# Kernel tuning notes

Measured on AMD Instinct MI355X. Metric: run time of the kernel, lower is better.

## Reference

```python
import jax, jax.numpy as jnp
import numpy as np

B, S, DIM, H = 2, 2048, 1024, 16
DK = DIM // H  # 64
NEG = -10000000000.0


def setup_inputs() -> dict:
    key = jax.random.key(0)
    k1, k2, k3, k4, k5, k6 = jax.random.split(key, 6)
    dec_xs = jax.random.normal(k1, (B, S, DIM), dtype=jnp.float32)
    enc_xs = jax.random.normal(k2, (B, S, DIM), dtype=jnp.float32)
    mask = jax.random.randint(k3, (B, S, S), 0, 2, dtype=jnp.int32)
    # torch Linear weights: out = x @ W.T, bias=False
    sc = 1.0 / np.sqrt(DIM)
    Wq = jax.random.normal(k4, (DIM, DIM), dtype=jnp.float32) * sc
    Wkv = jax.random.normal(k5, (2 * DIM, DIM), dtype=jnp.float32) * sc
    Wo = jax.random.normal(k6, (DIM, DIM), dtype=jnp.float32) * sc
    return {"dec_xs": dec_xs, "enc_xs": enc_xs, "Wq": Wq, "Wkv": Wkv, "Wo": Wo, "mask": mask}


def reference(dec_xs, enc_xs, Wq, Wkv, Wo, mask):
    b, s, dim = enc_xs.shape
    qs = dec_xs @ Wq.T                      # [b,s,dim]  (dropout inactive in eval)
    kv = enc_xs @ Wkv.T                     # [b,s,2*dim]
    ks, vs = jnp.split(kv, 2, axis=-1)
    # head layout: view(b, s, dk, h) -- heads LAST, as in the original
    qs = qs.reshape(b, s, DK, H)
    ks = ks.reshape(b, s, DK, H)
    vs = vs.reshape(b, s, DK, H)
    scores = jnp.einsum('bqdh,bkdh->bqkh', qs, ks) / np.sqrt(DK)
    scores = jnp.where(mask[..., None] == 0, NEG, scores)
    weights = jax.nn.softmax(scores, axis=-2)  # softmax over key axis
    out = jnp.einsum('bqkh,bkdh->bqdh', weights, vs).reshape(b, s, dim)
    return out @ Wo.T
```

## Files before the change

kernel.cpp:

```cpp
#include <hip/hip_runtime.h>
#include <hip/hip_bf16.h>

#define BB 2
#define SS 2048
#define DIMM 1024
#define HH 16
#define DKK 64
#define QSCALE 0.18033688011112042592f

using bf16 = __hip_bfloat16;
typedef __attribute__((ext_vector_type(8))) short v8s;
typedef __attribute__((ext_vector_type(4))) short v4s;
typedef __attribute__((ext_vector_type(4))) float f32x4;

__device__ __forceinline__ void cvt4(const float* __restrict__ s,
                                     bf16* __restrict__ d, int idx) {
  const float4 f = ((const float4*)s)[idx];
  bf16 t[4] = {__float2bfloat16(f.x), __float2bfloat16(f.y),
               __float2bfloat16(f.z), __float2bfloat16(f.w)};
  *(v4s*)(d + (size_t)idx * 4) = *(const v4s*)t;
}

__global__ __launch_bounds__(256) void convert_pack_kernel(
    const float* __restrict__ dec, const float* __restrict__ enc,
    const float* __restrict__ Wq, const float* __restrict__ Wkv,
    const float* __restrict__ Wo, const int* __restrict__ mask,
    bf16* __restrict__ decb, bf16* __restrict__ encb, bf16* __restrict__ Wqb,
    bf16* __restrict__ Wkvb, bf16* __restrict__ Wob,
    unsigned long long* __restrict__ mp) {
  const int gid = blockIdx.x * 256 + threadIdx.x;
  const int NT = 256 * 1024;
#pragma unroll
  for (int i = 0; i < 4; ++i) cvt4(dec, decb, gid + i * NT);
#pragma unroll
  for (int i = 0; i < 4; ++i) cvt4(enc, encb, gid + i * NT);
  cvt4(Wq, Wqb, gid);
#pragma unroll
  for (int i = 0; i < 2; ++i) cvt4(Wkv, Wkvb, gid + i * NT);
  cvt4(Wo, Wob, gid);
  const int lane = threadIdx.x & 63;
  const int wave_id = gid >> 6;
  for (int i = 0; i < 32; ++i) {
    const size_t w = (size_t)wave_id * 32 + i;
    const unsigned long long bm = __ballot(mask[w * 64 + lane] != 0);
    if (lane == 0) mp[w] = bm;
  }
}

__global__ __launch_bounds__(256) void proj_gemm_kernel(
    const bf16* __restrict__ decb, const bf16* __restrict__ encb,
    const bf16* __restrict__ Wqb, const bf16* __restrict__ Wkvb,
    bf16* __restrict__ Qr, bf16* __restrict__ Kr, bf16* __restrict__ Vt) {
  __shared__ __align__(16) bf16 As[128][72];
  __shared__ __align__(16) bf16 Bs[128][72];
  const int t = threadIdx.x;
  const int wave = t >> 6, lane = t & 63;
  const int quad = lane >> 4, l15 = lane & 15;
  const int wm = (wave >> 1) * 64, wn = (wave & 1) * 64;
  const int bx = blockIdx.x;
  const int kind = bx >> 3;
  const int g = bx & 7;
  const int m0 = blockIdx.y * 128;

  const bf16* Asrc = (kind == 0) ? decb : encb;
  const bf16* Wsrc = (kind == 0) ? Wqb : Wkvb;

  const int sr = t >> 2;
  const int sc = (t & 3) * 16;
  const int wr0 = sr * 16 + g * 2 + ((kind == 2) ? DIMM : 0);
  const int wr1 = sr * 16 + g * 2 + 1 + ((kind == 2) ? DIMM : 0);

  v8s apf[4], bpf[4];
  auto loadA = [&](int kc) {
    const bf16* p0 = Asrc + (size_t)(m0 + sr) * DIMM + kc + sc;
    apf[0] = ((const v8s*)p0)[0];
    apf[1] = ((const v8s*)p0)[1];
    const bf16* p1 = Asrc + (size_t)(m0 + sr + 64) * DIMM + kc + sc;
    apf[2] = ((const v8s*)p1)[0];
    apf[3] = ((const v8s*)p1)[1];
  };
  auto loadB = [&](int kc) {
    const bf16* q0 = Wsrc + (size_t)wr0 * DIMM + kc + sc;
    bpf[0] = ((const v8s*)q0)[0];
    bpf[1] = ((const v8s*)q0)[1];
    const bf16* q1 = Wsrc + (size_t)wr1 * DIMM + kc + sc;
    bpf[2] = ((const v8s*)q1)[0];
    bpf[3] = ((const v8s*)q1)[1];
  };

  f32x4 acc[4][4] = {};
  loadA(0);
  loadB(0);

  for (int kc = 0; kc < DIMM; kc += 64) {
    __syncthreads();
    *(v8s*)&As[sr][sc] = apf[0];
    *(v8s*)&As[sr][sc + 8] = apf[1];
    *(v8s*)&As[sr + 64][sc] = apf[2];
    *(v8s*)&As[sr + 64][sc + 8] = apf[3];
    *(v8s*)&Bs[sr][sc] = bpf[0];
    *(v8s*)&Bs[sr][sc + 8] = bpf[1];
    *(v8s*)&Bs[sr + 64][sc] = bpf[2];
    *(v8s*)&Bs[sr + 64][sc + 8] = bpf[3];
    if (kc + 64 < DIMM) {
      loadA(kc + 64);
      loadB(kc + 64);
    }
    __syncthreads();
#pragma unroll
    for (int ks = 0; ks < 2; ++ks) {
      v8s af[4], bfr[4];
#pragma unroll
      for (int i = 0; i < 4; ++i)
        af[i] = *(const v8s*)&As[wm + i * 16 + l15][ks * 32 + quad * 8];
#pragma unroll
      for (int j = 0; j < 4; ++j)
        bfr[j] = *(const v8s*)&Bs[wn + j * 16 + l15][ks * 32 + quad * 8];
#pragma unroll
      for (int i = 0; i < 4; ++i)
#pragma unroll
        for (int j = 0; j < 4; ++j)
          acc[i][j] = __builtin_amdgcn_mfma_f32_16x16x32_bf16(
              af[i], bfr[j], acc[i][j], 0, 0, 0);
    }
  }

#pragma unroll
  for (int i = 0; i < 4; ++i) {
#pragma unroll
    for (int r = 0; r < 4; ++r) {
      const int m = m0 + wm + i * 16 + quad * 4 + r;
#pragma unroll
      for (int j = 0; j < 4; ++j) {
        const int c = wn + j * 16 + l15;
        const int np = g * 128 + c;
        const float v = acc[i][j][r];
        if (kind == 0) {
          Qr[(size_t)m * DIMM + np] = __float2bfloat16(v * QSCALE);
        } else if (kind == 1) {
          Kr[(size_t)m * DIMM + np] = __float2bfloat16(v);
        } else {
          const int h = np >> 6, d = np & 63;
          const int b = m >> 11, s = m & (SS - 1);
          Vt[(((size_t)b * HH + h) * DKK + d) * SS + s] = __float2bfloat16(v);
        }
      }
    }
  }
}

__global__ __launch_bounds__(256) void out_gemm_kernel(
    const bf16* __restrict__ A, const bf16* __restrict__ W,
    float* __restrict__ out) {
  __shared__ __align__(16) bf16 As[128][72];
  __shared__ __align__(16) bf16 Bs[64][72];
  const int t = threadIdx.x;
  const int wave = t >> 6, lane = t & 63;
  const int quad = lane >> 4, l15 = lane & 15;
  const int wm = (wave >> 1) * 64, wn = (wave & 1) * 32;
  const int n0 = blockIdx.x * 64;
  const int m0 = blockIdx.y * 128;
  const int sr = t >> 2;
  const int sc = (t & 3) * 16;

  v8s ar[4], br[2];
  auto loadA = [&](int kc) {
#pragma unroll
    for (int rr = 0; rr < 2; ++rr) {
      const bf16* p = A + (size_t)(m0 + sr + rr * 64) * DIMM + kc + sc;
#pragma unroll
      for (int i = 0; i < 2; ++i) ar[rr * 2 + i] = ((const v8s*)p)[i];
    }
  };
  auto loadB = [&](int kc) {
    const bf16* p = W + (size_t)(n0 + sr) * DIMM + kc + sc;
#pragma unroll
    for (int i = 0; i < 2; ++i) br[i] = ((const v8s*)p)[i];
  };

  f32x4 acc[4][2] = {};
  loadA(0);
  loadB(0);
  for (int kc = 0; kc < DIMM; kc += 64) {
    __syncthreads();
#pragma unroll
    for (int rr = 0; rr < 2; ++rr) {
      *(v8s*)&As[sr + rr * 64][sc] = ar[rr * 2 + 0];
      *(v8s*)&As[sr + rr * 64][sc + 8] = ar[rr * 2 + 1];
    }
    *(v8s*)&Bs[sr][sc] = br[0];
    *(v8s*)&Bs[sr][sc + 8] = br[1];
    if (kc + 64 < DIMM) {
      loadA(kc + 64);
      loadB(kc + 64);
    }
    __syncthreads();
#pragma unroll
    for (int ks = 0; ks < 2; ++ks) {
      v8s af[4], bfr[2];
#pragma unroll
      for (int i = 0; i < 4; ++i)
        af[i] = *(const v8s*)&As[wm + i * 16 + l15][ks * 32 + quad * 8];
#pragma unroll
      for (int j = 0; j < 2; ++j)
        bfr[j] = *(const v8s*)&Bs[wn + j * 16 + l15][ks * 32 + quad * 8];
#pragma unroll
      for (int i = 0; i < 4; ++i)
#pragma unroll
        for (int j = 0; j < 2; ++j)
          acc[i][j] = __builtin_amdgcn_mfma_f32_16x16x32_bf16(
              af[i], bfr[j], acc[i][j], 0, 0, 0);
    }
  }

#pragma unroll
  for (int i = 0; i < 4; ++i) {
#pragma unroll
    for (int r = 0; r < 4; ++r) {
      const int m = m0 + wm + i * 16 + quad * 4 + r;
#pragma unroll
      for (int j = 0; j < 2; ++j) {
        const int n = n0 + wn + j * 16 + l15;
        out[(size_t)m * DIMM + n] = acc[i][j][r];
      }
    }
  }
}

__global__ __launch_bounds__(512) void attn_kernel(
    const bf16* __restrict__ Qr, const bf16* __restrict__ Kr,
    const bf16* __restrict__ Vt, const unsigned long long* __restrict__ mp,
    bf16* __restrict__ Ar) {
  __shared__ __align__(16) bf16 Ks[64][72];
  __shared__ __align__(16) bf16 Vs[64][72];
  __shared__ __align__(16) bf16 Ps[8][16][72];

  const int t = threadIdx.x;
  const int wave = t >> 6, lane = t & 63;
  const int quad = lane >> 4, l15 = lane & 15;

  const int bx = blockIdx.x;
  const int xcd = bx & 7, j = bx >> 3;
  const int g = (xcd << 2) | (j & 3);
  const int tile = j >> 2;
  const int h = g & 15, b = g >> 4;

  const int qw = tile * 128 + wave * 16;
  const size_t bhv = ((size_t)b * HH + h) * DKK;

  const bf16* qrow = Qr + ((size_t)(b * SS + qw + l15)) * DIMM + h * 64;
  const v8s aq0 = *(const v8s*)(qrow + quad * 8);
  const v8s aq1 = *(const v8s*)(qrow + 32 + quad * 8);

  f32x4 o[4] = {};
  float lsum[4] = {0.f, 0.f, 0.f, 0.f};

  const int id0 = t * 8;
  const int r0 = id0 >> 6, c0 = id0 & 63;

  for (int kt = 0; kt < 32; ++kt) {
    const int k0 = kt * 64;
    __syncthreads();
    {
      const bf16* kb = Kr + ((size_t)(b * SS + k0 + r0)) * DIMM + h * 64 + c0;
      *(v8s*)&Ks[r0][c0] = *(const v8s*)kb;
      *(v8s*)&Vs[r0][c0] = *(const v8s*)(Vt + (bhv + r0) * SS + k0 + c0);
    }
    __syncthreads();

    unsigned long long mw[4];
#pragma unroll
    for (int r = 0; r < 4; ++r)
      mw[r] = mp[((size_t)b * SS + qw + quad * 4 + r) * 32 + kt] >> l15;

    f32x4 sc[4];
#pragma unroll
    for (int n = 0; n < 4; ++n) {
      const v8s bk0 = *(const v8s*)&Ks[n * 16 + l15][quad * 8];
      const v8s bk1 = *(const v8s*)&Ks[n * 16 + l15][32 + quad * 8];
      f32x4 z = {0.f, 0.f, 0.f, 0.f};
      z = __builtin_amdgcn_mfma_f32_16x16x32_bf16(aq0, bk0, z, 0, 0, 0);
      sc[n] = __builtin_amdgcn_mfma_f32_16x16x32_bf16(aq1, bk1, z, 0, 0, 0);
    }

#pragma unroll
    for (int n = 0; n < 4; ++n)
#pragma unroll
      for (int r = 0; r < 4; ++r) {
        const bool keep = (mw[r] >> (n * 16)) & 1ULL;
        const float p = keep ? __builtin_amdgcn_exp2f(sc[n][r]) : 0.f;
        sc[n][r] = p;
        lsum[r] += p;
      }

#pragma unroll
    for (int n = 0; n < 4; ++n)
#pragma unroll
      for (int r = 0; r < 4; ++r)
        Ps[wave][quad * 4 + r][n * 16 + l15] = __float2bfloat16(sc[n][r]);
    const v8s ap0 = *(const v8s*)&Ps[wave][l15][quad * 8];
    const v8s ap1 = *(const v8s*)&Ps[wave][l15][32 + quad * 8];

#pragma unroll
    for (int n = 0; n < 4; ++n) {
      const v8s bv0 = *(const v8s*)&Vs[n * 16 + l15][quad * 8];
      const v8s bv1 = *(const v8s*)&Vs[n * 16 + l15][32 + quad * 8];
      o[n] = __builtin_amdgcn_mfma_f32_16x16x32_bf16(ap0, bv0, o[n], 0, 0, 0);
      o[n] = __builtin_amdgcn_mfma_f32_16x16x32_bf16(ap1, bv1, o[n], 0, 0, 0);
    }
  }

#pragma unroll
  for (int r = 0; r < 4; ++r) {
    float l = lsum[r];
    l += __shfl_xor(l, 1);
    l += __shfl_xor(l, 2);
    l += __shfl_xor(l, 4);
    l += __shfl_xor(l, 8);
    const float inv = 1.f / l;
    const size_t row = (size_t)b * SS + qw + quad * 4 + r;
#pragma unroll
    for (int n = 0; n < 4; ++n) {
      const int d = n * 16 + l15;
      Ar[row * DIMM + d * 16 + h] = __float2bfloat16(o[n][r] * inv);
    }
  }
}

extern "C" void kernel_launch(void* const* d_in, const int* in_sizes, int n_in,
                              void* d_out, int out_size, void* d_ws,
                              size_t ws_size, hipStream_t stream) {
  const float* dec = (const float*)d_in[0];
  const float* enc = (const float*)d_in[1];
  const float* Wq = (const float*)d_in[2];
  const float* Wkv = (const float*)d_in[3];
  const float* Wo = (const float*)d_in[4];
  const int* mask = (const int*)d_in[5];
  float* out = (float*)d_out;

  bf16* decb = (bf16*)d_out;
  bf16* Wqb = (bf16*)((char*)d_out + ((size_t)2 * SS * DIMM * 2));

  char* ws = (char*)d_ws;
  size_t off = 0;
  bf16* encb = (bf16*)(ws + off);
  bf16* Ar = (bf16*)(ws + off);   off += (size_t)2 * SS * DIMM * 2;
  bf16* Wkvb = (bf16*)(ws + off); off += (size_t)2 * DIMM * DIMM * 2;
  bf16* Wob = (bf16*)(ws + off);  off += (size_t)DIMM * DIMM * 2;
  bf16* Qr = (bf16*)(ws + off);   off += (size_t)2 * SS * DIMM * 2;
  bf16* Kr = (bf16*)(ws + off);   off += (size_t)2 * SS * DIMM * 2;
  bf16* Vt = (bf16*)(ws + off);   off += (size_t)2 * SS * DIMM * 2;
  unsigned long long* mp = (unsigned long long*)(ws + off);

  dim3 blk(256);
  convert_pack_kernel<<<dim3(1024), blk, 0, stream>>>(
      dec, enc, Wq, Wkv, Wo, mask, decb, encb, Wqb, Wkvb, Wob, mp);
  proj_gemm_kernel<<<dim3(24, 32), blk, 0, stream>>>(decb, encb, Wqb, Wkvb, Qr,
                                                     Kr, Vt);
  attn_kernel<<<dim3(512), dim3(512), 0, stream>>>(Qr, Kr, Vt, mp, Ar);
  out_gemm_kernel<<<dim3(16, 32), blk, 0, stream>>>(Ar, Wob, out);
}
```

Measured before the change: 282.8 us.

## Double-buffer K/V tiles in attention with register prefetch and one barrier

The attention kernel now keeps two LDS buffers each for the K and V tiles. The next tile is fetched from global memory into registers two iterations ahead and stored into the alternate buffer while the current tile is being consumed. This cuts the per-iteration barriers from two to one and hides global load latency behind the QK and PV MFMAs. The cost is more LDS per block, which could lower occupancy, plus extra registers for the prefetched vectors.

Result: faster. 274.3 us (-3.0%).

```diff
diff --git a/kernel.cpp b/kernel.cpp
--- a/kernel.cpp
+++ b/kernel.cpp
@@ -231,8 +231,8 @@
     const bf16* __restrict__ Qr, const bf16* __restrict__ Kr,
     const bf16* __restrict__ Vt, const unsigned long long* __restrict__ mp,
     bf16* __restrict__ Ar) {
-  __shared__ __align__(16) bf16 Ks[64][72];
-  __shared__ __align__(16) bf16 Vs[64][72];
+  __shared__ __align__(16) bf16 Ks[2][64][72];
+  __shared__ __align__(16) bf16 Vs[2][64][72];
   __shared__ __align__(16) bf16 Ps[8][16][72];
 
   const int t = threadIdx.x;
@@ -258,15 +258,31 @@
   const int id0 = t * 8;
   const int r0 = id0 >> 6, c0 = id0 & 63;
 
+  auto loadK = [&](int kt) {
+    return *(const v8s*)(Kr + ((size_t)(b * SS + kt * 64 + r0)) * DIMM +
+                         h * 64 + c0);
+  };
+  auto loadV = [&](int kt) {
+    return *(const v8s*)(Vt + (bhv + r0) * SS + kt * 64 + c0);
+  };
+
+  v8s kreg = loadK(0), vreg = loadV(0);
+  *(v8s*)&Ks[0][r0][c0] = kreg;
+  *(v8s*)&Vs[0][r0][c0] = vreg;
+  kreg = loadK(1);
+  vreg = loadV(1);
+
+  int p = 0;
   for (int kt = 0; kt < 32; ++kt) {
-    const int k0 = kt * 64;
-    __syncthreads();
-    {
-      const bf16* kb = Kr + ((size_t)(b * SS + k0 + r0)) * DIMM + h * 64 + c0;
-      *(v8s*)&Ks[r0][c0] = *(const v8s*)kb;
-      *(v8s*)&Vs[r0][c0] = *(const v8s*)(Vt + (bhv + r0) * SS + k0 + c0);
-    }
-    __syncthreads();
+    __syncthreads();
+    if (kt < 31) {
+      *(v8s*)&Ks[p ^ 1][r0][c0] = kreg;
+      *(v8s*)&Vs[p ^ 1][r0][c0] = vreg;
+      if (kt < 30) {
+        kreg = loadK(kt + 2);
+        vreg = loadV(kt + 2);
+      }
+    }
 
     unsigned long long mw[4];
 #pragma unroll
@@ -276,8 +292,8 @@
     f32x4 sc[4];
 #pragma unroll
     for (int n = 0; n < 4; ++n) {
-      const v8s bk0 = *(const v8s*)&Ks[n * 16 + l15][quad * 8];
-      const v8s bk1 = *(const v8s*)&Ks[n * 16 + l15][32 + quad * 8];
+      const v8s bk0 = *(const v8s*)&Ks[p][n * 16 + l15][quad * 8];
+      const v8s bk1 = *(const v8s*)&Ks[p][n * 16 + l15][32 + quad * 8];
       f32x4 z = {0.f, 0.f, 0.f, 0.f};
       z = __builtin_amdgcn_mfma_f32_16x16x32_bf16(aq0, bk0, z, 0, 0, 0);
       sc[n] = __builtin_amdgcn_mfma_f32_16x16x32_bf16(aq1, bk1, z, 0, 0, 0);
@@ -288,9 +304,9 @@
 #pragma unroll
       for (int r = 0; r < 4; ++r) {
         const bool keep = (mw[r] >> (n * 16)) & 1ULL;
-        const float p = keep ? __builtin_amdgcn_exp2f(sc[n][r]) : 0.f;
-        sc[n][r] = p;
-        lsum[r] += p;
+        const float pw = keep ? __builtin_amdgcn_exp2f(sc[n][r]) : 0.f;
+        sc[n][r] = pw;
+        lsum[r] += pw;
       }
 
 #pragma unroll
@@ -303,11 +319,12 @@
 
 #pragma unroll
     for (int n = 0; n < 4; ++n) {
-      const v8s bv0 = *(const v8s*)&Vs[n * 16 + l15][quad * 8];
-      const v8s bv1 = *(const v8s*)&Vs[n * 16 + l15][32 + quad * 8];
+      const v8s bv0 = *(const v8s*)&Vs[p][n * 16 + l15][quad * 8];
+      const v8s bv1 = *(const v8s*)&Vs[p][n * 16 + l15][32 + quad * 8];
       o[n] = __builtin_amdgcn_mfma_f32_16x16x32_bf16(ap0, bv0, o[n], 0, 0, 0);
       o[n] = __builtin_amdgcn_mfma_f32_16x16x32_bf16(ap1, bv1, o[n], 0, 0, 0);
     }
+    p ^= 1;
   }
 
 #pragma unroll
```
